# Optimization experiments

Measured on AMD Instinct MI355X. Metric: run time of the kernel, lower is better.

Reference implementation:

```python
import jax, jax.numpy as jnp
import numpy as np

B, N, IN, E, H, F = 64, 256, 128, 256, 8, 1024


def setup_inputs() -> dict:
    key = jax.random.key(0)
    ks = jax.random.split(key, 16)
    x = jax.random.normal(ks[0], (B, N, IN), jnp.float32)
    adj = (jax.random.uniform(ks[1], (B, N, N)) < 0.1).astype(jnp.float32)
    adj = jnp.maximum(adj, adj.transpose(0, 2, 1))  # symmetric 0/1 adjacency
    mask = jax.random.randint(ks[2], (B, N), 0, 2).astype(jnp.float32)
    dist = jax.random.normal(ks[3], (B, N, N), jnp.float32)

    def lin(k, i, o):
        return (jax.random.normal(k, (i, o), jnp.float32) / np.sqrt(i)).astype(jnp.float32)

    return dict(
        x=x, adj=adj, mask=mask, dist=dist,
        W1=lin(ks[4], IN, E), b1=jnp.zeros((E,), jnp.float32),
        W2=lin(ks[5], E, E), b2=jnp.zeros((E,), jnp.float32),
        W3=lin(ks[6], E, E), b3=jnp.zeros((E,), jnp.float32),
        ln1_g=jnp.ones((E,), jnp.float32), ln1_b=jnp.zeros((E,), jnp.float32),
        Wq=lin(ks[7], E, H * E), Wk=lin(ks[8], E, H * E), Wv=lin(ks[9], E, H * E),
        Wo=lin(ks[10], H * E, E), bo=jnp.zeros((E,), jnp.float32),
        ln2_g=jnp.ones((E,), jnp.float32), ln2_b=jnp.zeros((E,), jnp.float32),
        Wf1=lin(ks[11], E, F), bf1=jnp.zeros((F,), jnp.float32),
        Wf2=lin(ks[12], F, E), bf2=jnp.zeros((E,), jnp.float32),
    )


def _layernorm(x, g, b):
    m = x.mean(-1, keepdims=True)
    v = ((x - m) ** 2).mean(-1, keepdims=True)
    return (x - m) * jax.lax.rsqrt(v + 1e-5) * g + b


def reference(x, adj, mask, dist, W1, b1, W2, b2, W3, b3, ln1_g, ln1_b,
              Wq, Wk, Wv, Wo, bo, ln2_g, ln2_b, Wf1, bf1, Wf2, bf2):
    # --- DenseGCNConv normalization (add self-loops, sym-normalize) ---
    eye = jnp.eye(N, dtype=adj.dtype)
    A = adj * (1.0 - eye) + eye                      # fill_diag(adj, 1)
    dis = jax.lax.rsqrt(jnp.clip(A.sum(-1), 1.0, None))
    An = dis[:, :, None] * A * dis[:, None, :]       # D^-1/2 A D^-1/2, [B,N,N]
    m3 = mask[:, :, None]

    def gcn(h, W, b):
        return (jnp.einsum('bij,bjf->bif', An, h @ W) + b) * m3

    g1 = jax.nn.relu(gcn(x, W1, b1))
    g2 = jax.nn.relu(gcn(g1, W2, b2))
    g3 = jax.nn.relu(gcn(g2, W3, b3))
    gcn_res = g1 + g2 + g3

    # --- masked MHA with distance bias (head dim = E per head) ---
    h = _layernorm(gcn_res, ln1_g, ln1_b)
    mh = mask[:, None, :, None]                      # [B,1,N,1]
    q = (h @ Wq).reshape(B, N, H, E).transpose(0, 2, 1, 3) * mh
    k = (h @ Wk).reshape(B, N, H, E).transpose(0, 2, 1, 3) * mh
    v = (h @ Wv).reshape(B, N, H, E).transpose(0, 2, 1, 3) * mh
    a = jnp.einsum('bhne,bhme->bhnm', q * (E ** -0.5), k) + dist[:, None]
    am = (mask[:, :, None] * mask[:, None, :])[:, None]  # [B,1,N,N]
    a = jnp.where(am == 0, -1e9, a)
    a = jax.nn.softmax(a, axis=-1)
    a = jnp.where(am == 0, 0.0, a)
    y = jnp.einsum('bhnm,bhme->bhne', a, v).transpose(0, 2, 1, 3).reshape(B, N, H * E)
    y = (y @ Wo + bo) * m3
    att = gcn_res + y

    # --- FFN block ---
    f = _layernorm(att, ln2_g, ln2_b)
    f = (jax.nn.gelu(f @ Wf1 + bf1, approximate=False) @ Wf2 + bf2) * m3
    att = att + f
    return gcn_res + att
```

## Files before the change

kernel.cpp:

```cpp
#include <hip/hip_runtime.h>
#include <hip/hip_bf16.h>
#include <cmath>

#define BB 64
#define NNODES 256
#define INF_ 128
#define EE 256
#define HH 8
#define FFN 1024
#define BNROWS 16384

typedef __attribute__((ext_vector_type(8))) short short8;
typedef __attribute__((ext_vector_type(4))) float floatx4;
typedef __attribute__((ext_vector_type(4))) unsigned short ushort4v;

__device__ __forceinline__ float b2f(unsigned short u) {
  union { unsigned u32; float f; } w; w.u32 = ((unsigned)u) << 16; return w.f;
}
__device__ __forceinline__ unsigned short f2b(float f) {
  union { float f; unsigned u32; } w; w.f = f;
  unsigned r = w.u32 + 0x7FFFu + ((w.u32 >> 16) & 1u);
  return (unsigned short)(r >> 16);
}
__device__ __forceinline__ float gelu_f(float x) {
  const float z = 0.7978845608028654f * (x + 0.044715f * x * x * x);
  const float e = __expf(2.0f * z);
  const float th = (e - 1.0f) / (e + 1.0f);
  return 0.5f * x * (1.0f + th);
}

typedef const __attribute__((address_space(1))) void GV;
typedef __attribute__((address_space(3))) void LV;

__device__ __forceinline__ void gl_lds16(const unsigned short* g,
                                         unsigned short* l, int lane) {
#if __has_builtin(__builtin_amdgcn_global_load_lds)
  __builtin_amdgcn_global_load_lds((GV*)g, (LV*)l, 16, 0, 0);
#else
  *(short8*)(l + lane * 8) = *(const short8*)g;
#endif
}

struct PackArgs {
  const float* src[12];
  unsigned short* dst[12];
  int R[12], C[12];
  int start[13];
};

__launch_bounds__(256)
__global__ void pack_kernel(PackArgs a)
{
  __shared__ float tile[32][33];
  const int bid = blockIdx.x;
  int j = 0;
  while (bid >= a.start[j + 1]) j++;
  const int lb = bid - a.start[j];
  const float* src = a.src[j];
  unsigned short* dst = a.dst[j];
  const int R = a.R[j], C = a.C[j];

  if (C == 0) {
    const int i = (lb * 256 + threadIdx.x) * 4;
    if (i >= R) return;
    floatx4 v = *(const floatx4*)(src + i);
    ushort4v o;
    #pragma unroll
    for (int k = 0; k < 4; k++) o[k] = f2b(v[k]);
    *(ushort4v*)(dst + i) = o;
    return;
  }
  const int tpr = C >> 5;
  const int c0 = (lb % tpr) * 32, r0 = (lb / tpr) * 32;
  const int tx = threadIdx.x & 31, ty = threadIdx.x >> 5;
  #pragma unroll
  for (int i = ty; i < 32; i += 8)
    tile[i][tx] = src[(long long)(r0 + i) * C + c0 + tx];
  __syncthreads();
  #pragma unroll
  for (int i = ty; i < 32; i += 8)
    dst[(long long)(c0 + i) * R + r0 + tx] = f2b(tile[tx][i]);
}

__global__ void deg_kernel(const float* __restrict__ adj,
                           float* __restrict__ dis)
{
  const int g = blockIdx.x * 4 + (threadIdx.x >> 6);
  const int lane = threadIdx.x & 63;
  const int i = g & 255;
  floatx4 v = *(const floatx4*)(adj + (long long)g * 256 + lane * 4);
  float s = 0.f;
  #pragma unroll
  for (int jj = 0; jj < 4; jj++) {
    const int j = lane * 4 + jj;
    s += (j == i) ? 1.0f : v[jj];
  }
  #pragma unroll
  for (int off = 32; off > 0; off >>= 1) s += __shfl_xor(s, off);
  if (lane == 0) dis[g] = 1.0f / sqrtf(fmaxf(s, 1.0f));
}

__global__ void an_kernel(const float* __restrict__ adj,
                          const float* __restrict__ dis,
                          unsigned short* __restrict__ An)
{
  const long long base = ((long long)blockIdx.x * 256 + threadIdx.x) * 4;
  const int rowg = (int)(base >> 8);
  const int i = rowg & 255;
  const int brow = rowg & ~255;
  const int j0 = (int)(base & 255);
  const float di = dis[rowg];
  floatx4 v = *(const floatx4*)(adj + base);
  ushort4v o;
  #pragma unroll
  for (int jj = 0; jj < 4; jj++) {
    const int j = j0 + jj;
    const float a = (j == i) ? 1.0f : v[jj];
    o[jj] = f2b(di * dis[brow + j] * a);
  }
  *(ushort4v*)(An + base) = o;
}

__launch_bounds__(512, 4)
__global__ void gemm_kernel(const unsigned short* __restrict__ A, int lda,
                            long long sAo, long long sAi,
                            const unsigned short* __restrict__ Bm, int ldb,
                            long long sBo, long long sBi,
                            void* __restrict__ Cv, int ldc,
                            long long sCo, long long sCi,
                            int K, int zshift, int mode, int flag,
                            const float* __restrict__ aux1,
                            const float* __restrict__ mask,
                            float* __restrict__ gcn,
                            void* __restrict__ aux2)
{
  __shared__ __align__(16) unsigned short sA[16384];
  __shared__ __align__(16) unsigned short sB[16384];

  const int t = threadIdx.x;
  const int z = blockIdx.z;
  const int zi = z & ((1 << zshift) - 1);
  const int zb = z >> zshift;
  const int m0 = blockIdx.x * 128;
  const int n0 = blockIdx.y * 128;
  A  += zb * sAo + zi * sAi;
  Bm += zb * sBo + zi * sBi;
  const long long cbase = zb * sCo + zi * sCi;

  const int lane = t & 63;
  const int w = t >> 6;
  const int wm = w >> 2, wn = w & 3;
  const int lm = lane & 15, qd = lane >> 4;

  floatx4 acc[4][2] = {};

  const int sub = lane >> 4;
  const int qs  = lane & 15;
  const unsigned short* pA[4];
  const unsigned short* pB[4];
  #pragma unroll
  for (int i = 0; i < 4; i++) {
    const int d = w * 4 + i;
    const int r = d * 4 + sub;
    const int co = (qs ^ (r & 7)) * 8;
    pA[i] = A + (long long)(m0 + r) * lda + co;
    pB[i] = Bm + (long long)(n0 + r) * ldb + co;
  }

  for (int kk = 0; kk < K; kk += 128) {
    #pragma unroll
    for (int i = 0; i < 4; i++) {
      gl_lds16(pA[i] + kk, &sA[(w * 4 + i) * 512], lane);
      gl_lds16(pB[i] + kk, &sB[(w * 4 + i) * 512], lane);
    }
    __syncthreads();

    #pragma unroll
    for (int ks = 0; ks < 4; ks++) {
      short8 af[4], bg[2];
      const int q = ks * 4 + qd;
      #pragma unroll
      for (int mi = 0; mi < 4; mi++) {
        const int r = wm * 64 + mi * 16 + lm;
        af[mi] = *(const short8*)&sA[r * 128 + ((q ^ (r & 7)) * 8)];
      }
      #pragma unroll
      for (int ni = 0; ni < 2; ni++) {
        const int r = wn * 32 + ni * 16 + lm;
        bg[ni] = *(const short8*)&sB[r * 128 + ((q ^ (r & 7)) * 8)];
      }
      #pragma unroll
      for (int mi = 0; mi < 4; mi++)
        #pragma unroll
        for (int ni = 0; ni < 2; ni++)
          acc[mi][ni] = __builtin_amdgcn_mfma_f32_16x16x32_bf16(
              af[mi], bg[ni], acc[mi][ni], 0, 0, 0);
    }
    __syncthreads();
  }

  #pragma unroll
  for (int mi = 0; mi < 4; mi++) {
    const int row0 = m0 + wm * 64 + mi * 16 + qd * 4;
    #pragma unroll
    for (int ni = 0; ni < 2; ni++) {
      const int col = n0 + wn * 32 + ni * 16 + lm;
      floatx4 a = acc[mi][ni];
      if (mode == 0) {
        float* Cf = (float*)Cv;
        #pragma unroll
        for (int r = 0; r < 4; r++)
          Cf[cbase + (long long)(row0 + r) * ldc + col] = a[r];
      } else if (mode == 1) {
        unsigned short* Cb = (unsigned short*)Cv;
        #pragma unroll
        for (int r = 0; r < 4; r++)
          Cb[cbase + (long long)(row0 + r) * ldc + col] = f2b(a[r]);
      } else if (mode == 2) {
        float* Cf = (float*)Cv;
        #pragma unroll
        for (int r = 0; r < 4; r++)
          Cf[cbase + (long long)(row0 + r) * ldc + col] += a[r];
      } else if (mode == 3) {
        unsigned short* Cb = (unsigned short*)Cv;
        const float bv = aux1[col];
        #pragma unroll
        for (int r = 0; r < 4; r++)
          Cb[cbase + (long long)(row0 + r) * ldc + col] = f2b(gelu_f(a[r] + bv));
      } else if (mode == 5) {
        const int b = row0 >> 8, n = row0 & 255;
        ushort4v o;
        #pragma unroll
        for (int r = 0; r < 4; r++) o[r] = f2b(a[r]);
        *(ushort4v*)((unsigned short*)Cv + (long long)b * 65536 + col * 256 + n) = o;
      } else if (mode == 8) {
        float* Cf = (float*)Cv;
        const float* attf = (const float*)aux2;
        const float bv = aux1[col];
        #pragma unroll
        for (int r = 0; r < 4; r++) {
          const long long idx = (long long)(row0 + r) * 256 + col;
          Cf[idx] = gcn[idx] + attf[idx] + (a[r] + bv) * mask[row0 + r];
        }
      } else if (mode == 9) {
        const int token = zb * 256 + col;
        const float m = mask[token];
        ushort4v o; floatx4 g;
        #pragma unroll
        for (int r = 0; r < 4; r++) {
          const float v = fmaxf((a[r] + aux1[row0 + r]) * m, 0.f);
          o[r] = f2b(v); g[r] = v;
        }
        *(ushort4v*)((unsigned short*)Cv + (long long)token * 256 + row0) = o;
        float* gp = gcn + (long long)token * 256 + row0;
        if (flag) { floatx4 old = *(const floatx4*)gp; g += old; }
        *(floatx4*)gp = g;
      } else if (mode == 12) {
        float* Cf = (float*)Cv;
        const float bv = aux1[col];
        #pragma unroll
        for (int r = 0; r < 4; r++) {
          const long long idx = (long long)(row0 + r) * 256 + col;
          Cf[idx] = gcn[idx] + (a[r] + bv) * mask[row0 + r];
        }
      } else if (mode == 13) {
        unsigned short* Cb = (unsigned short*)Cv;
        #pragma unroll
        for (int r = 0; r < 4; r++)
          Cb[cbase + (long long)(row0 + r) * ldc + col] = f2b(a[r] * 0.0625f);
      } else {
        if (col < 2048) {
          unsigned short* Cb = (unsigned short*)Cv;
          #pragma unroll
          for (int r = 0; r < 4; r++)
            Cb[(long long)(row0 + r) * 2048 + col] = f2b(a[r]);
        } else {
          const int z2 = (row0 >> 8) * 8 + ((col >> 8) - 8);
          const int e = col & 255, n = row0 & 255;
          ushort4v o;
          #pragma unroll
          for (int r = 0; r < 4; r++) o[r] = f2b(a[r]);
          *(ushort4v*)((unsigned short*)aux2 + (long long)z2 * 65536 + e * 256 + n) = o;
        }
      }
    }
  }
}

__launch_bounds__(512, 2)
__global__ void attn_kernel(unsigned short* __restrict__ QP,
                            const unsigned short* __restrict__ HBF,
                            const unsigned short* __restrict__ VT,
                            const unsigned short* __restrict__ DSTB,
                            const float* __restrict__ mask)
{
  __shared__ __align__(16) unsigned short sQ[8192];
  __shared__ __align__(16) unsigned short sKV[16896];
  __shared__ float redm[4][128];
  __shared__ float reds[4][128];

  const int bi = blockIdx.x;
  const int z  = (bi >> 4) * 8 + (bi & 7);
  const int mt = (bi & 15) >> 3;
  const int b  = z >> 3, h = z & 7;
  const int t = threadIdx.x, lane = t & 63, w = t >> 6;
  const int wm = w >> 2, wn = w & 3;
  const int lm = lane & 15, qd = lane >> 4;
  const int m0 = mt * 128;

  unsigned short* Qm = QP + ((long long)(b * 256 + m0)) * 2048 + h * 256;
  const unsigned short* Hb = HBF + (long long)b * 65536;
  const unsigned short* Vb = VT + (long long)z * 65536;
  const unsigned short* db = DSTB + (long long)b * 65536;
  const float* maskb = mask + b * 256;

  const int rin = lane >> 3;
  const int qs  = lane & 7;

  floatx4 S[4][4] = {};
  for (int c = 0; c < 4; c++) {
    const int e0 = c * 64;
    #pragma unroll
    for (int i = 0; i < 2; i++) {
      const int d = w * 2 + i;
      const int r = d * 8 + rin;
      gl_lds16(Qm + (long long)r * 2048 + e0 + ((qs ^ (r & 7)) * 8),
               &sQ[d * 512], lane);
    }
    #pragma unroll
    for (int i = 0; i < 4; i++) {
      const int d = w * 4 + i;
      const int r = d * 8 + rin;
      gl_lds16(Hb + (long long)r * 256 + e0 + ((qs ^ (r & 7)) * 8),
               &sKV[d * 512], lane);
    }
    __syncthreads();
    #pragma unroll
    for (int ks = 0; ks < 2; ks++) {
      short8 af[4], bg4[4];
      const int o = ks * 4 + qd;
      #pragma unroll
      for (int mi = 0; mi < 4; mi++) {
        const int r = wm * 64 + mi * 16 + lm;
        af[mi] = *(const short8*)&sQ[r * 64 + ((o ^ (r & 7)) * 8)];
      }
      #pragma unroll
      for (int ni = 0; ni < 4; ni++) {
        const int r = wn * 64 + ni * 16 + lm;
        bg4[ni] = *(const short8*)&sKV[r * 64 + ((o ^ (r & 7)) * 8)];
      }
      #pragma unroll
      for (int mi = 0; mi < 4; mi++)
        #pragma unroll
        for (int ni = 0; ni < 4; ni++)
          S[mi][ni] = __builtin_amdgcn_mfma_f32_16x16x32_bf16(
              af[mi], bg4[ni], S[mi][ni], 0, 0, 0);
    }
    __syncthreads();
  }

  #pragma unroll
  for (int i = 0; i < 4; i++) {
    const int d = w * 4 + i;
    const int r = d * 8 + rin;
    gl_lds16(Vb + (long long)r * 256 + ((qs ^ (r & 7)) * 8),
             &sKV[d * 512], lane);
  }

  float mk[4];
  #pragma unroll
  for (int ni = 0; ni < 4; ni++) mk[ni] = maskb[wn * 64 + ni * 16 + lm];

  float lred[4][4];
  #pragma unroll
  for (int mi = 0; mi < 4; mi++) {
    #pragma unroll
    for (int r = 0; r < 4; r++) {
      const int row = wm * 64 + mi * 16 + qd * 4 + r;
      const float mq = maskb[m0 + row];
      float mx = -3e38f;
      #pragma unroll
      for (int ni = 0; ni < 4; ni++) {
        const int col = wn * 64 + ni * 16 + lm;
        const float dv = b2f(db[(long long)(m0 + row) * 256 + col]);
        const float v = (mq != 0.f && mk[ni] != 0.f) ? (S[mi][ni][r] + dv) : -1e9f;
        S[mi][ni][r] = v;
        mx = fmaxf(mx, v);
      }
      lred[mi][r] = mx;
    }
  }
  #pragma unroll
  for (int off = 1; off < 16; off <<= 1)
    #pragma unroll
    for (int mi = 0; mi < 4; mi++)
      #pragma unroll
      for (int r = 0; r < 4; r++)
        lred[mi][r] = fmaxf(lred[mi][r], __shfl_xor(lred[mi][r], off));
  if (lm == 0)
    #pragma unroll
    for (int mi = 0; mi < 4; mi++)
      #pragma unroll
      for (int r = 0; r < 4; r++)
        redm[wn][wm * 64 + mi * 16 + qd * 4 + r] = lred[mi][r];
  __syncthreads();

  #pragma unroll
  for (int mi = 0; mi < 4; mi++) {
    #pragma unroll
    for (int r = 0; r < 4; r++) {
      const int row = wm * 64 + mi * 16 + qd * 4 + r;
      const float gmax = fmaxf(fmaxf(redm[0][row], redm[1][row]),
                               fmaxf(redm[2][row], redm[3][row]));
      float s = 0.f;
      #pragma unroll
      for (int ni = 0; ni < 4; ni++) {
        const float e = __expf(S[mi][ni][r] - gmax);
        S[mi][ni][r] = e;
        s += e;
      }
      lred[mi][r] = s;
    }
  }
  #pragma unroll
  for (int off = 1; off < 16; off <<= 1)
    #pragma unroll
    for (int mi = 0; mi < 4; mi++)
      #pragma unroll
      for (int r = 0; r < 4; r++)
        lred[mi][r] += __shfl_xor(lred[mi][r], off);
  if (lm == 0)
    #pragma unroll
    for (int mi = 0; mi < 4; mi++)
      #pragma unroll
      for (int r = 0; r < 4; r++)
        reds[wn][wm * 64 + mi * 16 + qd * 4 + r] = lred[mi][r];
  __syncthreads();

  #pragma unroll
  for (int mi = 0; mi < 4; mi++) {
    #pragma unroll
    for (int r = 0; r < 4; r++) {
      const int row = wm * 64 + mi * 16 + qd * 4 + r;
      const float gs = reds[0][row] + reds[1][row] + reds[2][row] + reds[3][row];
      const float inv = 1.0f / gs;
      #pragma unroll
      for (int ni = 0; ni < 4; ni++) S[mi][ni][r] *= inv;
    }
  }

  floatx4 Y[4][4] = {};
  for (int c = 0; c < 4; c++) {
    if (wn == c) {
      #pragma unroll
      for (int mi = 0; mi < 4; mi++)
        #pragma unroll
        for (int r = 0; r < 4; r++) {
          const int row = wm * 64 + mi * 16 + qd * 4 + r;
          #pragma unroll
          for (int ni = 0; ni < 4; ni++) {
            const int kl = ni * 16 + lm;
            const int slot = (kl >> 3) ^ (row & 7);
            sQ[row * 64 + slot * 8 + (kl & 7)] = f2b(S[mi][ni][r]);
          }
        }
    }
    __syncthreads();
    #pragma unroll
    for (int ks = 0; ks < 2; ks++) {
      short8 af[4], bg4[4];
      const int o = ks * 4 + qd;
      #pragma unroll
      for (int mi = 0; mi < 4; mi++) {
        const int r = wm * 64 + mi * 16 + lm;
        af[mi] = *(const short8*)&sQ[r * 64 + ((o ^ (r & 7)) * 8)];
      }
      #pragma unroll
      for (int ni = 0; ni < 4; ni++) {
        const int r = wn * 64 + ni * 16 + lm;
        bg4[ni] = *(const short8*)&sKV[r * 64 + ((o ^ (r & 7)) * 8)];
      }
      #pragma unroll
      for (int mi = 0; mi < 4; mi++)
        #pragma unroll
        for (int ni = 0; ni < 4; ni++)
          Y[mi][ni] = __builtin_amdgcn_mfma_f32_16x16x32_bf16(
              af[mi], bg4[ni], Y[mi][ni], 0, 0, 0);
    }
    __syncthreads();
    if (c < 3) {
      #pragma unroll
      for (int i = 0; i < 4; i++) {
        const int d = w * 4 + i;
        const int r = d * 8 + rin;
        gl_lds16(Vb + (long long)r * 256 + (c + 1) * 64 + ((qs ^ (r & 7)) * 8),
                 &sKV[d * 512], lane);
      }
    }
  }

  #pragma unroll
  for (int half = 0; half < 2; half++) {
    __syncthreads();
    if (wm == half) {
      #pragma unroll
      for (int mi = 0; mi < 4; mi++)
        #pragma unroll
        for (int ni = 0; ni < 4; ni++) {
          const int col = wn * 64 + ni * 16 + lm;
          #pragma unroll
          for (int r = 0; r < 4; r++) {
            const int rl = mi * 16 + qd * 4 + r;
            sKV[rl * 264 + col] = f2b(Y[mi][ni][r]);
          }
        }
    }
    __syncthreads();
    #pragma unroll
    for (int it = 0; it < 4; it++) {
      const int idx = it * 512 + t;
      const int row = idx >> 5, u = idx & 31;
      short8 v = *(const short8*)&sKV[row * 264 + u * 8];
      *(short8*)(Qm + (long long)(half * 64 + row) * 2048 + u * 8) = v;
    }
  }
}

__global__ void ln_kernel(const float* __restrict__ X,
                          const float* __restrict__ gam,
                          const float* __restrict__ bet,
                          unsigned short* __restrict__ out)
{
  const int g = blockIdx.x * 4 + (threadIdx.x >> 6);
  const int lane = threadIdx.x & 63;
  floatx4 v = *(const floatx4*)(X + (long long)g * 256 + lane * 4);
  float s = v[0] + v[1] + v[2] + v[3];
  float sq = v[0]*v[0] + v[1]*v[1] + v[2]*v[2] + v[3]*v[3];
  #pragma unroll
  for (int off = 32; off > 0; off >>= 1) {
    s  += __shfl_xor(s, off);
    sq += __shfl_xor(sq, off);
  }
  const float mean = s * (1.0f / 256.0f);
  const float var = sq * (1.0f / 256.0f) - mean * mean;
  const float rs = 1.0f / sqrtf(var + 1e-5f);
  ushort4v o;
  #pragma unroll
  for (int jj = 0; jj < 4; jj++) {
    const int c = lane * 4 + jj;
    o[jj] = f2b((v[jj] - mean) * rs * gam[c] + bet[c]);
  }
  *(ushort4v*)(out + (long long)g * 256 + lane * 4) = o;
}

static inline void launch_gemm(hipStream_t st, int M, int N, int batch,
    const void* A, int lda, long long sAo, long long sAi,
    const void* B, int ldb, long long sBo, long long sBi,
    void* C, int ldc, long long sCo, long long sCi,
    int K, int zshift, int mode, int flag,
    const float* aux1, const float* mask, float* gcn, void* aux2)
{
  dim3 grid(M / 128, N / 128, batch), blk(512);
  gemm_kernel<<<grid, blk, 0, st>>>(
      (const unsigned short*)A, lda, sAo, sAi,
      (const unsigned short*)B, ldb, sBo, sBi,
      C, ldc, sCo, sCi, K, zshift, mode, flag, aux1, mask, gcn, aux2);
}

extern "C" void kernel_launch(void* const* d_in, const int* in_sizes, int n_in,
                              void* d_out, int out_size, void* d_ws, size_t ws_size,
                              hipStream_t stream)
{
  (void)in_sizes; (void)n_in; (void)out_size;
  const float* x    = (const float*)d_in[0];
  const float* adj  = (const float*)d_in[1];
  const float* mask = (const float*)d_in[2];
  const float* dist = (const float*)d_in[3];
  const float* W1   = (const float*)d_in[4];
  const float* b1   = (const float*)d_in[5];
  const float* W2   = (const float*)d_in[6];
  const float* b2   = (const float*)d_in[7];
  const float* W3   = (const float*)d_in[8];
  const float* b3   = (const float*)d_in[9];
  const float* ln1g = (const float*)d_in[10];
  const float* ln1b = (const float*)d_in[11];
  const float* Wq   = (const float*)d_in[12];
  const float* Wk   = (const float*)d_in[13];
  const float* Wv   = (const float*)d_in[14];
  const float* Wo   = (const float*)d_in[15];
  const float* bo   = (const float*)d_in[16];
  const float* ln2g = (const float*)d_in[17];
  const float* ln2b = (const float*)d_in[18];
  const float* Wf1  = (const float*)d_in[19];
  const float* bf1  = (const float*)d_in[20];
  const float* Wf2  = (const float*)d_in[21];
  const float* bf2  = (const float*)d_in[22];

  char* w = (char*)d_ws;
  auto alloc = [&](size_t sz) { void* p = (void*)w; w += sz; return p; };
  unsigned short* W1T   = (unsigned short*)alloc(65536);
  unsigned short* W2T   = (unsigned short*)alloc(131072);
  unsigned short* W3T   = (unsigned short*)alloc(131072);
  unsigned short* ABH   = (unsigned short*)alloc(1048576);
  unsigned short* WVT   = (unsigned short*)alloc(1048576);
  unsigned short* WOT   = (unsigned short*)alloc(1048576);
  unsigned short* WF1T  = (unsigned short*)alloc(524288);
  unsigned short* WF2T  = (unsigned short*)alloc(524288);
  unsigned short* WQb   = (unsigned short*)alloc(1048576);
  unsigned short* WKb   = (unsigned short*)alloc(1048576);
  unsigned short* XBF   = (unsigned short*)alloc(4194304);
  unsigned short* DSTB  = (unsigned short*)alloc(8388608);
  float*          GCN   = (float*)         alloc(16777216);
  float*          U     = (float*)         alloc(16777216);
  unsigned short* HBF   = (unsigned short*)alloc(8388608);
  float*          DIS   = (float*)         alloc(65536);
  char* scratch = (char*)alloc(134217728);
  if ((size_t)(w - (char*)d_ws) > ws_size) return;
  unsigned short* AN  = (unsigned short*)scratch;
  unsigned short* TT  = (unsigned short*)(scratch + 8388608);
  unsigned short* GBF = (unsigned short*)(scratch + 16777216);
  unsigned short* QPB = (unsigned short*)scratch;
  unsigned short* VT  = (unsigned short*)(scratch + 67108864);
  unsigned short* FFB = (unsigned short*)scratch;

  PackArgs pa;
  const float* srcs[11] = {W1, W2, W3, Wv, Wo, Wf1, Wf2, x, Wq, Wk, dist};
  unsigned short* dsts[11] = {W1T, W2T, W3T, WVT, WOT, WF1T, WF2T, XBF, WQb, WKb, DSTB};
  const int Rs[11] = {128, 256, 256, 256, 2048, 256, 1024,
                      BNROWS * INF_, EE * HH * EE, EE * HH * EE, BB * 65536};
  const int Cs[11] = {256, 256, 256, 2048, 256, 1024, 256, 0, 0, 0, 0};
  const int sts[12] = {0, 32, 96, 160, 672, 1184, 1440, 1696, 3744, 4256, 4768, 8864};
  for (int j = 0; j < 11; j++) {
    pa.src[j] = srcs[j]; pa.dst[j] = dsts[j]; pa.R[j] = Rs[j]; pa.C[j] = Cs[j];
  }
  for (int j = 0; j < 12; j++) pa.start[j] = sts[j];
  pack_kernel<<<8864, 256, 0, stream>>>(pa);

  deg_kernel<<<4096, 256, 0, stream>>>(adj, DIS);
  an_kernel<<<4096, 256, 0, stream>>>(adj, DIS, AN);

  launch_gemm(stream, 256, 256, 8, WKb, 2048, 256, 0, WQb, 2048, 256, 0,
              ABH, 256, 65536, 0, 256, 0, 13, 0, nullptr, nullptr, nullptr, nullptr);

  launch_gemm(stream, BNROWS, EE, 1, XBF, 128, 0,0, W1T, 128, 0,0,
              TT, 256, 0,0, 128, 0, 5, 0, nullptr, nullptr, nullptr, nullptr);
  launch_gemm(stream, 256, 256, BB, TT, 256, 65536,0, AN, 256, 65536,0,
              GBF, 256, 0,0, 256, 0, 9, 0, b1, mask, GCN, nullptr);
  launch_gemm(stream, BNROWS, EE, 1, GBF, 256, 0,0, W2T, 256, 0,0,
              TT, 256, 0,0, 256, 0, 5, 0, nullptr, nullptr, nullptr, nullptr);
  launch_gemm(stream, 256, 256, BB, TT, 256, 65536,0, AN, 256, 65536,0,
              GBF, 256, 0,0, 256, 0, 9, 1, b2, mask, GCN, nullptr);
  launch_gemm(stream, BNROWS, EE, 1, GBF, 256, 0,0, W3T, 256, 0,0,
              TT, 256, 0,0, 256, 0, 5, 0, nullptr, nullptr, nullptr, nullptr);
  launch_gemm(stream, 256, 256, BB, TT, 256, 65536,0, AN, 256, 65536,0,
              GBF, 256, 0,0, 256, 0, 9, 1, b3, mask, GCN, nullptr);

  ln_kernel<<<4096, 256, 0, stream>>>(GCN, ln1g, ln1b, HBF);

  launch_gemm(stream, BNROWS, 4096, 1, HBF, 256, 0,0, ABH, 256, 0,0,
              QPB, 2048, 0,0, 256, 0, 15, 0, nullptr, nullptr, nullptr, VT);
  attn_kernel<<<1024, 512, 0, stream>>>(QPB, HBF, VT, DSTB, mask);
  launch_gemm(stream, BNROWS, EE, 1, QPB, 2048, 0,0, WOT, 2048, 0,0,
              U, 256, 0,0, 2048, 0, 12, 0, bo, mask, GCN, nullptr);

  ln_kernel<<<4096, 256, 0, stream>>>(U, ln2g, ln2b, HBF);
  launch_gemm(stream, BNROWS, FFN, 1, HBF, 256, 0,0, WF1T, 256, 0,0,
              FFB, 1024, 0,0, 256, 0, 3, 0, bf1, nullptr, nullptr, nullptr);
  launch_gemm(stream, BNROWS, EE, 1, FFB, 1024, 0,0, WF2T, 1024, 0,0,
              d_out, 256, 0,0, 1024, 0, 8, 0, bf2, mask, GCN, U);
}
```

Before: 496.8 us.

## Restructure attention kernel: register-resident Q, double-buffered K/V, full-row P in LDS

The attention kernel now loads the full 128x256 Q tile into LDS once and holds it in registers. K and V chunks are double-buffered so the next chunk's global-to-LDS load overlaps the current MFMA work. The QK^T phase uses a new 4x2 wave tiling over 32-row blocks, and the normalized probability matrix is written once into a full 128x256 LDS buffer instead of per-chunk rewrites with extra barriers. LDS use rises to about 128KB per block, so the two-blocks-per-CU occupancy target may not be met. The block-to-(batch, head, tile) mapping is also reordered so blocks that share a batch's inputs run close together.

```diff
diff --git a/kernel.cpp b/kernel.cpp
--- a/kernel.cpp
+++ b/kernel.cpp
@@ -294,19 +294,23 @@
                             const unsigned short* __restrict__ DSTB,
                             const float* __restrict__ mask)
 {
-  __shared__ __align__(16) unsigned short sQ[8192];
-  __shared__ __align__(16) unsigned short sKV[16896];
-  __shared__ float redm[4][128];
-  __shared__ float reds[4][128];
+  __shared__ __align__(16) unsigned short sP[32768];
+  __shared__ __align__(16) unsigned short sKV[32768];
+  __shared__ float redm[2][128];
+  __shared__ float reds[2][128];
 
   const int bi = blockIdx.x;
-  const int z  = (bi >> 4) * 8 + (bi & 7);
-  const int mt = (bi & 15) >> 3;
-  const int b  = z >> 3, h = z & 7;
+  const int x = bi & 7, sdx = bi >> 3;
+  const int h = sdx & 7;
+  const int p = (sdx >> 3) * 8 + x;
+  const int b = p >> 1, mt = p & 1;
+  const int m0 = mt * 128;
+  const int z = b * 8 + h;
+
   const int t = threadIdx.x, lane = t & 63, w = t >> 6;
-  const int wm = w >> 2, wn = w & 3;
   const int lm = lane & 15, qd = lane >> 4;
-  const int m0 = mt * 128;
+  const int wm4 = w >> 1, wn2 = w & 1;
+  const int wmP = w >> 2, wnP = w & 3;
 
   unsigned short* Qm = QP + ((long long)(b * 256 + m0)) * 2048 + h * 256;
   const unsigned short* Hb = HBF + (long long)b * 65536;
@@ -314,200 +318,213 @@
   const unsigned short* db = DSTB + (long long)b * 65536;
   const float* maskb = mask + b * 256;
 
-  const int rin = lane >> 3;
-  const int qs  = lane & 7;
-
-  floatx4 S[4][4] = {};
-  for (int c = 0; c < 4; c++) {
-    const int e0 = c * 64;
-    #pragma unroll
-    for (int i = 0; i < 2; i++) {
-      const int d = w * 2 + i;
-      const int r = d * 8 + rin;
-      gl_lds16(Qm + (long long)r * 2048 + e0 + ((qs ^ (r & 7)) * 8),
-               &sQ[d * 512], lane);
-    }
-    #pragma unroll
-    for (int i = 0; i < 4; i++) {
-      const int d = w * 4 + i;
-      const int r = d * 8 + rin;
-      gl_lds16(Hb + (long long)r * 256 + e0 + ((qs ^ (r & 7)) * 8),
-               &sKV[d * 512], lane);
-    }
-    __syncthreads();
-    #pragma unroll
-    for (int ks = 0; ks < 2; ks++) {
-      short8 af[4], bg4[4];
-      const int o = ks * 4 + qd;
-      #pragma unroll
-      for (int mi = 0; mi < 4; mi++) {
-        const int r = wm * 64 + mi * 16 + lm;
-        af[mi] = *(const short8*)&sQ[r * 64 + ((o ^ (r & 7)) * 8)];
-      }
-      #pragma unroll
-      for (int ni = 0; ni < 4; ni++) {
-        const int r = wn * 64 + ni * 16 + lm;
-        bg4[ni] = *(const short8*)&sKV[r * 64 + ((o ^ (r & 7)) * 8)];
-      }
-      #pragma unroll
-      for (int mi = 0; mi < 4; mi++)
-        #pragma unroll
-        for (int ni = 0; ni < 4; ni++)
-          S[mi][ni] = __builtin_amdgcn_mfma_f32_16x16x32_bf16(
-              af[mi], bg4[ni], S[mi][ni], 0, 0, 0);
-    }
-    __syncthreads();
-  }
-
+  const int rin2 = lane >> 5, qs32 = lane & 31;
+  const int rin8 = lane >> 3, qs8  = lane & 7;
+
+  #pragma unroll
+  for (int i = 0; i < 8; i++) {
+    const int d = w * 8 + i;
+    const int r = d * 2 + rin2;
+    gl_lds16(Qm + (long long)r * 2048 + ((qs32 ^ (r & 7)) * 8), &sP[d * 512], lane);
+  }
   #pragma unroll
   for (int i = 0; i < 4; i++) {
     const int d = w * 4 + i;
-    const int r = d * 8 + rin;
-    gl_lds16(Vb + (long long)r * 256 + ((qs ^ (r & 7)) * 8),
-             &sKV[d * 512], lane);
-  }
-
-  float mk[4];
-  #pragma unroll
-  for (int ni = 0; ni < 4; ni++) mk[ni] = maskb[wn * 64 + ni * 16 + lm];
-
-  float lred[4][4];
-  #pragma unroll
-  for (int mi = 0; mi < 4; mi++) {
+    const int r = d * 2 + rin2;
+    gl_lds16(Hb + (long long)r * 256 + ((qs32 ^ (r & 7)) * 8), &sKV[d * 512], lane);
+  }
+  __syncthreads();
+
+  short8 afq[2][8];
+  #pragma unroll
+  for (int mi = 0; mi < 2; mi++) {
+    const int r = wm4 * 32 + mi * 16 + lm;
+    #pragma unroll
+    for (int ks = 0; ks < 8; ks++) {
+      const int q = ks * 4 + qd;
+      afq[mi][ks] = *(const short8*)&sP[r * 256 + ((q ^ (r & 7)) * 8)];
+    }
+  }
+
+  floatx4 S[4][2][2] = {};
+  #pragma unroll
+  for (int c = 0; c < 4; c++) {
+    const int cur = (c & 1) * 16384;
+    if (c < 3) {
+      #pragma unroll
+      for (int i = 0; i < 4; i++) {
+        const int d = w * 4 + i;
+        const int r = d * 2 + rin2;
+        gl_lds16(Hb + (long long)((c + 1) * 64 + r) * 256 + ((qs32 ^ (r & 7)) * 8),
+                 &sKV[(cur ^ 16384) + d * 512], lane);
+      }
+    }
+    #pragma unroll
+    for (int ks = 0; ks < 8; ks++) {
+      const int q = ks * 4 + qd;
+      short8 bg[2];
+      #pragma unroll
+      for (int ni = 0; ni < 2; ni++) {
+        const int kk = wn2 * 32 + ni * 16 + lm;
+        bg[ni] = *(const short8*)&sKV[cur + kk * 256 + ((q ^ (kk & 7)) * 8)];
+      }
+      #pragma unroll
+      for (int mi = 0; mi < 2; mi++)
+        #pragma unroll
+        for (int ni = 0; ni < 2; ni++)
+          S[c][mi][ni] = __builtin_amdgcn_mfma_f32_16x16x32_bf16(
+              afq[mi][ks], bg[ni], S[c][mi][ni], 0, 0, 0);
+    }
+    __syncthreads();
+  }
+
+  #pragma unroll
+  for (int i = 0; i < 4; i++) {
+    const int d = w * 4 + i;
+    const int r = d * 8 + rin8;
+    gl_lds16(Vb + (long long)r * 256 + ((qs8 ^ (r & 7)) * 8), &sKV[d * 512], lane);
+  }
+
+  float mkv[4][2];
+  #pragma unroll
+  for (int c = 0; c < 4; c++)
+    #pragma unroll
+    for (int ni = 0; ni < 2; ni++)
+      mkv[c][ni] = maskb[c * 64 + wn2 * 32 + ni * 16 + lm];
+
+  float lred[2][4];
+  #pragma unroll
+  for (int mi = 0; mi < 2; mi++) {
     #pragma unroll
     for (int r = 0; r < 4; r++) {
-      const int row = wm * 64 + mi * 16 + qd * 4 + r;
+      const int row = wm4 * 32 + mi * 16 + qd * 4 + r;
       const float mq = maskb[m0 + row];
       float mx = -3e38f;
       #pragma unroll
-      for (int ni = 0; ni < 4; ni++) {
-        const int col = wn * 64 + ni * 16 + lm;
-        const float dv = b2f(db[(long long)(m0 + row) * 256 + col]);
-        const float v = (mq != 0.f && mk[ni] != 0.f) ? (S[mi][ni][r] + dv) : -1e9f;
-        S[mi][ni][r] = v;
-        mx = fmaxf(mx, v);
-      }
+      for (int c = 0; c < 4; c++)
+        #pragma unroll
+        for (int ni = 0; ni < 2; ni++) {
+          const int col = c * 64 + wn2 * 32 + ni * 16 + lm;
+          const float dv = b2f(db[(long long)(m0 + row) * 256 + col]);
+          const float v = (mq != 0.f && mkv[c][ni] != 0.f) ? (S[c][mi][ni][r] + dv) : -1e9f;
+          S[c][mi][ni][r] = v;
+          mx = fmaxf(mx, v);
+        }
       lred[mi][r] = mx;
     }
   }
   #pragma unroll
   for (int off = 1; off < 16; off <<= 1)
     #pragma unroll
-    for (int mi = 0; mi < 4; mi++)
+    for (int mi = 0; mi < 2; mi++)
       #pragma unroll
       for (int r = 0; r < 4; r++)
         lred[mi][r] = fmaxf(lred[mi][r], __shfl_xor(lred[mi][r], off));
   if (lm == 0)
     #pragma unroll
-    for (int mi = 0; mi < 4; mi++)
+    for (int mi = 0; mi < 2; mi++)
       #pragma unroll
       for (int r = 0; r < 4; r++)
-        redm[wn][wm * 64 + mi * 16 + qd * 4 + r] = lred[mi][r];
+        redm[wn2][wm4 * 32 + mi * 16 + qd * 4 + r] = lred[mi][r];
   __syncthreads();
 
   #pragma unroll
-  for (int mi = 0; mi < 4; mi++) {
+  for (int mi = 0; mi < 2; mi++) {
     #pragma unroll
     for (int r = 0; r < 4; r++) {
-      const int row = wm * 64 + mi * 16 + qd * 4 + r;
-      const float gmax = fmaxf(fmaxf(redm[0][row], redm[1][row]),
-                               fmaxf(redm[2][row], redm[3][row]));
-      float s = 0.f;
-      #pragma unroll
-      for (int ni = 0; ni < 4; ni++) {
-        const float e = __expf(S[mi][ni][r] - gmax);
-        S[mi][ni][r] = e;
-        s += e;
-      }
-      lred[mi][r] = s;
+      const int row = wm4 * 32 + mi * 16 + qd * 4 + r;
+      const float gmax = fmaxf(redm[0][row], redm[1][row]);
+      float ss = 0.f;
+      #pragma unroll
+      for (int c = 0; c < 4; c++)
+        #pragma unroll
+        for (int ni = 0; ni < 2; ni++) {
+          const float e = __expf(S[c][mi][ni][r] - gmax);
+          S[c][mi][ni][r] = e;
+          ss += e;
+        }
+      lred[mi][r] = ss;
     }
   }
   #pragma unroll
   for (int off = 1; off < 16; off <<= 1)
     #pragma unroll
-    for (int mi = 0; mi < 4; mi++)
+    for (int mi = 0; mi < 2; mi++)
       #pragma unroll
       for (int r = 0; r < 4; r++)
         lred[mi][r] += __shfl_xor(lred[mi][r], off);
   if (lm == 0)
     #pragma unroll
-    for (int mi = 0; mi < 4; mi++)
+    for (int mi = 0; mi < 2; mi++)
       #pragma unroll
       for (int r = 0; r < 4; r++)
-        reds[wn][wm * 64 + mi * 16 + qd * 4 + r] = lred[mi][r];
+        reds[wn2][wm4 * 32 + mi * 16 + qd * 4 + r] = lred[mi][r];
   __syncthreads();
 
   #pragma unroll
-  for (int mi = 0; mi < 4; mi++) {
+  for (int mi = 0; mi < 2; mi++)
     #pragma unroll
     for (int r = 0; r < 4; r++) {
-      const int row = wm * 64 + mi * 16 + qd * 4 + r;
-      const float gs = reds[0][row] + reds[1][row] + reds[2][row] + reds[3][row];
-      const float inv = 1.0f / gs;
-      #pragma unroll
-      for (int ni = 0; ni < 4; ni++) S[mi][ni][r] *= inv;
-    }
-  }
+      const int row = wm4 * 32 + mi * 16 + qd * 4 + r;
+      const float inv = 1.0f / (reds[0][row] + reds[1][row]);
+      #pragma unroll
+      for (int c = 0; c < 4; c++)
+        #pragma unroll
+        for (int ni = 0; ni < 2; ni++) {
+          const int col = c * 64 + wn2 * 32 + ni * 16 + lm;
+          sP[row * 256 + (((col >> 3) ^ (row & 7)) * 8) + (col & 7)] =
+              f2b(S[c][mi][ni][r] * inv);
+        }
+    }
+  __syncthreads();
 
   floatx4 Y[4][4] = {};
+  #pragma unroll
   for (int c = 0; c < 4; c++) {
-    if (wn == c) {
-      #pragma unroll
-      for (int mi = 0; mi < 4; mi++)
-        #pragma unroll
-        for (int r = 0; r < 4; r++) {
-          const int row = wm * 64 + mi * 16 + qd * 4 + r;
-          #pragma unroll
-          for (int ni = 0; ni < 4; ni++) {
-            const int kl = ni * 16 + lm;
-            const int slot = (kl >> 3) ^ (row & 7);
-            sQ[row * 64 + slot * 8 + (kl & 7)] = f2b(S[mi][ni][r]);
-          }
-        }
-    }
-    __syncthreads();
+    const int cur = (c & 1) * 16384;
+    if (c < 3) {
+      #pragma unroll
+      for (int i = 0; i < 4; i++) {
+        const int d = w * 4 + i;
+        const int r = d * 8 + rin8;
+        gl_lds16(Vb + (long long)r * 256 + (c + 1) * 64 + ((qs8 ^ (r & 7)) * 8),
+                 &sKV[(cur ^ 16384) + d * 512], lane);
+      }
+    }
     #pragma unroll
     for (int ks = 0; ks < 2; ks++) {
-      short8 af[4], bg4[4];
       const int o = ks * 4 + qd;
+      const int qP = c * 8 + o;
+      short8 af[4], bg[4];
       #pragma unroll
       for (int mi = 0; mi < 4; mi++) {
-        const int r = wm * 64 + mi * 16 + lm;
-        af[mi] = *(const short8*)&sQ[r * 64 + ((o ^ (r & 7)) * 8)];
+        const int r = wmP * 64 + mi * 16 + lm;
+        af[mi] = *(const short8*)&sP[r * 256 + ((qP ^ (r & 7)) * 8)];
       }
       #pragma unroll
       for (int ni = 0; ni < 4; ni++) {
-        const int r = wn * 64 + ni * 16 + lm;
-        bg4[ni] = *(const short8*)&sKV[r * 64 + ((o ^ (r & 7)) * 8)];
+        const int e = wnP * 64 + ni * 16 + lm;
+        bg[ni] = *(const short8*)&sKV[cur + e * 64 + ((o ^ (e & 7)) * 8)];
       }
       #pragma unroll
       for (int mi = 0; mi < 4; mi++)
         #pragma unroll
         for (int ni = 0; ni < 4; ni++)
           Y[mi][ni] = __builtin_amdgcn_mfma_f32_16x16x32_bf16(
-              af[mi], bg4[ni], Y[mi][ni], 0, 0, 0);
+              af[mi], bg[ni], Y[mi][ni], 0, 0, 0);
     }
     __syncthreads();
-    if (c < 3) {
-      #pragma unroll
-      for (int i = 0; i < 4; i++) {
-        const int d = w * 4 + i;
-        const int r = d * 8 + rin;
-        gl_lds16(Vb + (long long)r * 256 + (c + 1) * 64 + ((qs ^ (r & 7)) * 8),
-                 &sKV[d * 512], lane);
-      }
-    }
   }
 
   #pragma unroll
   for (int half = 0; half < 2; half++) {
     __syncthreads();
-    if (wm == half) {
+    if (wmP == half) {
       #pragma unroll
       for (int mi = 0; mi < 4; mi++)
         #pragma unroll
         for (int ni = 0; ni < 4; ni++) {
-          const int col = wn * 64 + ni * 16 + lm;
+          const int col = wnP * 64 + ni * 16 + lm;
           #pragma unroll
           for (int r = 0; r < 4; r++) {
             const int rl = mi * 16 + qd * 4 + r;
```

Result: faster. 478.2 us (-3.7%).
